# Optimization experiments

Measured on AMD Instinct MI355X. Metric: run time of the kernel, lower is better.

The kernel has to match this reference:

```python
import jax, jax.numpy as jnp
import numpy as np

N_NODES = 25000
N_EDGES = 400000
ATOM_DIM = 39
EDGE_DIM = 10
FP = 128


def setup_inputs() -> dict:
    key = jax.random.key(0)
    ks = iter(jax.random.split(key, 40))
    def rn(shape, scale=0.1):
        return (jax.random.normal(next(ks), shape, dtype=jnp.float32) * scale)
    inp = {
        'x': jax.random.normal(next(ks), (N_NODES, ATOM_DIM), dtype=jnp.float32),
        'edge_index': jax.random.randint(next(ks), (2, N_EDGES), 0, N_NODES, dtype=jnp.int32),
        'edge_attr': jax.random.normal(next(ks), (N_EDGES, EDGE_DIM), dtype=jnp.float32),
        # layer 0 (step=0): atom_fc + neighbor_fc + align/attend/GRU
        'l0_atom_fc_w': rn((FP, ATOM_DIM)), 'l0_atom_fc_b': rn((FP,)),
        'l0_neighbor_fc_w': rn((FP, ATOM_DIM + EDGE_DIM)), 'l0_neighbor_fc_b': rn((FP,)),
        'l0_align_w': rn((1, 2 * FP)), 'l0_align_b': rn((1,)),
        'l0_attend_w': rn((FP, FP)), 'l0_attend_b': rn((FP,)),
        'l0_w_ih': rn((3 * FP, FP)), 'l0_w_hh': rn((3 * FP, FP)),
        'l0_b_ih': rn((3 * FP,)), 'l0_b_hh': rn((3 * FP,)),
        # layer 1 (step=1): align/attend/GRU only
        'l1_align_w': rn((1, 2 * FP)), 'l1_align_b': rn((1,)),
        'l1_attend_w': rn((FP, FP)), 'l1_attend_b': rn((FP,)),
        'l1_w_ih': rn((3 * FP, FP)), 'l1_w_hh': rn((3 * FP, FP)),
        'l1_b_ih': rn((3 * FP,)), 'l1_b_hh': rn((3 * FP,)),
    }
    return inp


def _lrelu(v):
    return jax.nn.leaky_relu(v, negative_slope=0.01)


def _gru_cell(inp, h, w_ih, w_hh, b_ih, b_hh):
    # torch.nn.GRUCell math
    gi = inp @ w_ih.T + b_ih
    gh = h @ w_hh.T + b_hh
    i_r, i_z, i_n = jnp.split(gi, 3, axis=-1)
    h_r, h_z, h_n = jnp.split(gh, 3, axis=-1)
    r = jax.nn.sigmoid(i_r + h_r)
    z = jax.nn.sigmoid(i_z + h_z)
    n = jnp.tanh(i_n + r * h_n)
    return (1.0 - z) * n + z * h


def _segment_softmax(e, idx, num_segments):
    # PyG torch_geometric.utils.softmax: per-segment max-shifted exp / (sum + 1e-16)
    m = jax.ops.segment_max(e, idx, num_segments=num_segments)
    ex = jnp.exp(e - m[idx])
    s = jax.ops.segment_sum(ex, idx, num_segments=num_segments)
    return ex / (s[idx] + 1e-16)


def _edge_block(x_i, x_j, src, dst, n_nodes, aw, ab, tw, tb, w_ih, w_hh, b_ih, b_hh):
    # align -> segment softmax (keyed by source index, as in the torch code) -> attend -> GRU -> scatter-add
    evu = _lrelu(jnp.concatenate([x_i, x_j], axis=-1) @ aw.T + ab)      # [E,1]
    avu = _segment_softmax(evu, src, n_nodes)                            # [E,1]
    c = jax.nn.elu(avu * (x_i @ tw.T + tb))                              # [E,FP]; dropout is identity in eval
    h = _gru_cell(c, x_i, w_ih, w_hh, b_ih, b_hh)                        # [E,FP]
    return jax.ops.segment_sum(h, dst, num_segments=n_nodes)            # [N,FP] default 'add' aggregation


def reference(x, edge_index, edge_attr,
              l0_atom_fc_w, l0_atom_fc_b, l0_neighbor_fc_w, l0_neighbor_fc_b,
              l0_align_w, l0_align_b, l0_attend_w, l0_attend_b,
              l0_w_ih, l0_w_hh, l0_b_ih, l0_b_hh,
              l1_align_w, l1_align_b, l1_attend_w, l1_attend_b,
              l1_w_ih, l1_w_hh, l1_b_ih, l1_b_hh):
    src, dst = edge_index[0], edge_index[1]   # PyG flow source_to_target: x_j=x[src], x_i=x[dst]
    n_nodes = x.shape[0]
    # --- layer 0 (step == 0) ---
    x_i = _lrelu(x[dst] @ l0_atom_fc_w.T + l0_atom_fc_b)
    x_j = _lrelu(jnp.concatenate([x[src], edge_attr], axis=-1) @ l0_neighbor_fc_w.T + l0_neighbor_fc_b)
    x = _edge_block(x_i, x_j, src, dst, n_nodes,
                    l0_align_w, l0_align_b, l0_attend_w, l0_attend_b,
                    l0_w_ih, l0_w_hh, l0_b_ih, l0_b_hh)
    # --- layer 1 (step == 1) ---
    x_i = x[dst]
    x_j = x[src]
    x = _edge_block(x_i, x_j, src, dst, n_nodes,
                    l1_align_w, l1_align_b, l1_attend_w, l1_attend_b,
                    l1_w_ih, l1_w_hh, l1_b_ih, l1_b_hh)
    return x
```

## Files before the change

### kernel.cpp

```cpp
#include <hip/hip_runtime.h>
#include <math.h>

#define NN 25000
#define NE 400000
#define NINF -1e30f

typedef __attribute__((ext_vector_type(8))) short bf16x8;
typedef __attribute__((ext_vector_type(4))) float f32x4;

__device__ __forceinline__ float lrelu(float x){ return x > 0.f ? x : 0.01f*x; }
__device__ __forceinline__ float elu1(float x){ return x > 0.f ? x : (__expf(x)-1.f); }
__device__ __forceinline__ float sigm(float x){ return 1.f/(1.f+__expf(-x)); }
__device__ __forceinline__ float tanh_fast(float x){ float e=__expf(2.f*x); return 1.f - 2.f/(e+1.f); }
__device__ __forceinline__ short f2bf(float f){
    union { float f; unsigned u; } v; v.f = f;
    unsigned r = v.u + 0x7fff + ((v.u >> 16) & 1);
    return (short)(r >> 16);
}
__device__ __forceinline__ float bf2f(short s){
    union { unsigned u; float f; } v; v.u = ((unsigned)(unsigned short)s) << 16;
    return v.f;
}
__device__ __forceinline__ unsigned cvtpk_bf16(float lo, float hi){
    unsigned r;
    asm volatile("v_cvt_pk_bf16_f32 %0, %1, %2" : "=v"(r) : "v"(lo), "v"(hi));
    return r;
}

__global__ __launch_bounds__(256) void k_pack8(
    const float* __restrict__ w0, const float* __restrict__ w1,
    const float* __restrict__ w2, const float* __restrict__ w3,
    const float* __restrict__ w4, const float* __restrict__ w5,
    const float* __restrict__ w6, const float* __restrict__ w7,
    short* __restrict__ o0, short* __restrict__ o1, short* __restrict__ o2,
    short* __restrict__ o3, short* __restrict__ o4, short* __restrict__ o5,
    short* __restrict__ o6, short* __restrict__ o7)
{
    int b = blockIdx.x;
    if (b < 896){
        const float* w; short* o; int idx;
        if      (b < 192){ w=w0; o=o0; idx = b*256; }
        else if (b < 384){ w=w1; o=o1; idx = (b-192)*256; }
        else if (b < 576){ w=w2; o=o2; idx = (b-384)*256; }
        else if (b < 768){ w=w3; o=o3; idx = (b-576)*256; }
        else if (b < 832){ w=w4; o=o4; idx = (b-768)*256; }
        else             { w=w5; o=o5; idx = (b-832)*256; }
        idx += threadIdx.x;
        int i    = idx & 7;
        int lane = (idx >> 3) & 63;
        int ks   = (idx >> 9) & 3;
        int tile = idx >> 11;
        int row  = tile*16 + (lane & 15);
        int k    = ks*32 + ((lane >> 4) << 3) + i;
        o[idx] = f2bf(w[row*128 + k]);
    } else {
        const float* w; short* o; int idx; int pitch;
        if (b < 928){ w=w6; o=o6; idx = (b-896)*256; pitch = 39; }
        else        { w=w7; o=o7; idx = (b-928)*256; pitch = 49; }
        idx += threadIdx.x;
        int i    = idx & 7;
        int lane = (idx >> 3) & 63;
        int ks   = (idx >> 9) & 1;
        int tile = idx >> 10;
        int row  = tile*16 + (lane & 15);
        int k    = ks*32 + ((lane >> 4) << 3) + i;
        o[idx] = (k < 39) ? f2bf(w[row*pitch + k]) : (short)0;
    }
}

__global__ __launch_bounds__(256) void k_hist2(const int* __restrict__ src,
                                               const int* __restrict__ dst,
                                               unsigned* __restrict__ hd,
                                               unsigned* __restrict__ hs)
{
    int e = blockIdx.x*256 + threadIdx.x;
    if (e < NE){
        atomicAdd(&hd[dst[e]], 1u);
        atomicAdd(&hs[src[e]], 1u);
    }
}

__global__ __launch_bounds__(1024) void k_scan2(
    const unsigned* __restrict__ hd, unsigned* __restrict__ cd,
    const unsigned* __restrict__ hs, unsigned* __restrict__ cs,
    int* __restrict__ srcptr)
{
    __shared__ unsigned ps[1024];
    const int issrc = blockIdx.x;
    const unsigned* h = issrc ? hs : hd;
    unsigned* c = issrc ? cs : cd;
    const int t = threadIdx.x;
    unsigned loc[25]; unsigned sum = 0;
    const int base = t*25;
    #pragma unroll
    for (int i=0;i<25;i++){ int n=base+i; unsigned v=(n<NN)?h[n]:0u; loc[i]=sum; sum+=v; }
    ps[t]=sum; __syncthreads();
    for (int off=1; off<1024; off<<=1){
        unsigned v = (t>=off)? ps[t-off] : 0u;
        __syncthreads();
        ps[t] += v;
        __syncthreads();
    }
    unsigned bex = (t==0)? 0u : ps[t-1];
    #pragma unroll
    for (int i=0;i<25;i++){
        int n=base+i;
        if (n<NN){
            unsigned off = bex + loc[i];
            c[n] = off;
            if (issrc) srcptr[n] = (int)off;
        }
    }
    if (issrc && t==1023) srcptr[NN] = NE;
}

__global__ __launch_bounds__(256) void k_scatter2(
    const int* __restrict__ src, const int* __restrict__ dst,
    unsigned* __restrict__ cd, unsigned* __restrict__ cs,
    int* __restrict__ se_dst, int* __restrict__ inv_dst,
    int* __restrict__ se2_id, int* __restrict__ se2_dst)
{
    int e = blockIdx.x*256 + threadIdx.x;
    if (e < NE){
        int d = dst[e], s = src[e];
        unsigned p = atomicAdd(&cd[d], 1u);
        se_dst[p] = d;
        inv_dst[e] = (int)p;
        unsigned q = atomicAdd(&cs[s], 1u);
        se2_id[q] = e;
        se2_dst[q] = d;
    }
}

__global__ __launch_bounds__(512) void k_l0_prep(
    const float* __restrict__ x,
    const float* __restrict__ ba, const float* __restrict__ bn,
    const float* __restrict__ aw,
    const short* __restrict__ wap, const short* __restrict__ wnp,
    const short* __restrict__ twp, const float* __restrict__ tb,
    const short* __restrict__ whhp, const float* __restrict__ bhh,
    short* __restrict__ A16, short* __restrict__ B16, float* __restrict__ di,
    short* __restrict__ T16, short* __restrict__ GH16)
{
    __shared__ short x_lds[64*72];
    __shared__ __align__(16) char A_lds[64*272];
    const int t = threadIdx.x;
    const int base = blockIdx.x << 6;
    for (int idx = t; idx < 64*64; idx += 512){
        int r = idx >> 6, k = idx & 63;
        int node = base + r;
        float v = (k < 39 && node < NN) ? x[(size_t)node*39 + k] : 0.f;
        x_lds[r*72 + k] = f2bf(v);
    }
    __syncthreads();
    const int w = t >> 6, lane = t & 63;
    const int l15 = lane & 15, lhi = lane >> 4;
    const int jb = w*16 + l15;
    f32x4 Aacc[4], Bacc[4];
    #pragma unroll
    for (int m=0; m<4; ++m){ Aacc[m] = (f32x4){0,0,0,0}; Bacc[m] = (f32x4){0,0,0,0}; }
    #pragma unroll
    for (int ks=0; ks<2; ++ks){
        bf16x8 af[4];
        #pragma unroll
        for (int m=0; m<4; ++m)
            af[m] = *(const bf16x8*)&x_lds[(m*16+l15)*72 + ks*32 + lhi*8];
        bf16x8 wfA = *(const bf16x8*)(wap + (size_t)((w*2 + ks)*64 + lane)*8);
        bf16x8 wfB = *(const bf16x8*)(wnp + (size_t)((w*2 + ks)*64 + lane)*8);
        #pragma unroll
        for (int m=0; m<4; ++m){
            Aacc[m] = __builtin_amdgcn_mfma_f32_16x16x32_bf16(af[m], wfA, Aacc[m], 0, 0, 0);
            Bacc[m] = __builtin_amdgcn_mfma_f32_16x16x32_bf16(af[m], wfB, Bacc[m], 0, 0, 0);
        }
    }
    {
        float bav = ba[jb], bnv = bn[jb];
        #pragma unroll
        for (int m=0; m<4; ++m){
            #pragma unroll
            for (int reg=0; reg<4; ++reg){
                int e = m*16 + lhi*4 + reg;
                int node = base + e;
                float avv = lrelu(Aacc[m][reg] + bav);
                short ab16 = f2bf(avv);
                *(short*)(A_lds + e*272 + jb*2) = ab16;
                if (node < NN){
                    A16[(size_t)node*128 + jb] = ab16;
                    B16[(size_t)node*128 + jb] = f2bf(Bacc[m][reg] + bnv);
                }
            }
        }
    }
    __syncthreads();
    {
        float a0 = aw[lane], a1 = aw[64+lane];
        for (int i=0;i<8;++i){
            int r = w*8 + i;
            int node = base + r;
            float v0 = bf2f(*(const short*)(A_lds + r*272 + lane*2));
            float v1 = bf2f(*(const short*)(A_lds + r*272 + 128 + lane*2));
            float pa = v0*a0 + v1*a1;
            #pragma unroll
            for (int off=32; off; off>>=1) pa += __shfl_xor(pa, off);
            if (lane==0 && node<NN) di[node] = pa;
        }
    }
    f32x4 Tacc[4], gh[4][3];
    {
        float tbv = tb[jb];
        #pragma unroll
        for (int m=0; m<4; ++m) Tacc[m] = (f32x4){tbv, tbv, tbv, tbv};
        #pragma unroll
        for (int g=0; g<3; ++g){
            float bv = bhh[g*128 + jb];
            #pragma unroll
            for (int m=0; m<4; ++m) gh[m][g] = (f32x4){bv, bv, bv, bv};
        }
    }
    #pragma unroll
    for (int ks=0; ks<4; ++ks){
        bf16x8 af[4];
        #pragma unroll
        for (int m=0; m<4; ++m)
            af[m] = *(const bf16x8*)(A_lds + (m*16+l15)*272 + ks*64 + (lhi<<4));
        bf16x8 tf = *(const bf16x8*)(twp + (size_t)((w*4 + ks)*64 + lane)*8);
        #pragma unroll
        for (int m=0; m<4; ++m)
            Tacc[m] = __builtin_amdgcn_mfma_f32_16x16x32_bf16(af[m], tf, Tacc[m], 0, 0, 0);
        #pragma unroll
        for (int g=0; g<3; ++g){
            bf16x8 wf = *(const bf16x8*)(whhp + (size_t)(((g*8+w)*4 + ks)*64 + lane)*8);
            #pragma unroll
            for (int m=0; m<4; ++m)
                gh[m][g] = __builtin_amdgcn_mfma_f32_16x16x32_bf16(af[m], wf, gh[m][g], 0, 0, 0);
        }
    }
    #pragma unroll
    for (int m=0; m<4; ++m){
        #pragma unroll
        for (int reg=0; reg<4; ++reg){
            int node = base + m*16 + lhi*4 + reg;
            if (node < NN){
                T16[(size_t)node*128 + jb]        = f2bf(Tacc[m][reg]);
                GH16[(size_t)node*384 + jb]       = f2bf(gh[m][0][reg]);
                GH16[(size_t)node*384 + 128 + jb] = f2bf(gh[m][1][reg]);
                GH16[(size_t)node*384 + 256 + jb] = f2bf(gh[m][2][reg]);
            }
        }
    }
}

__global__ __launch_bounds__(512) void k_l1_prep(
    const float* __restrict__ out0, const float* __restrict__ aw,
    const short* __restrict__ twp, const float* __restrict__ tb,
    const short* __restrict__ whhp, const float* __restrict__ bhh,
    short* __restrict__ x16, float* __restrict__ di, float* __restrict__ dj,
    short* __restrict__ T16, short* __restrict__ GH16)
{
    __shared__ __align__(16) char x_lds[64*272];
    const int t = threadIdx.x;
    const int base = blockIdx.x << 6;
    {
        int r = t >> 3, c0 = (t & 7) * 16;
        int node = base + r;
        int nc = node < NN ? node : NN-1;
        const float4* sp = (const float4*)(out0 + (size_t)nc*128 + c0);
        float4 f0 = sp[0], f1 = sp[1], f2 = sp[2], f3 = sp[3];
        union { short s[16]; int4 v[2]; } u;
        u.s[0]=f2bf(f0.x); u.s[1]=f2bf(f0.y); u.s[2]=f2bf(f0.z); u.s[3]=f2bf(f0.w);
        u.s[4]=f2bf(f1.x); u.s[5]=f2bf(f1.y); u.s[6]=f2bf(f1.z); u.s[7]=f2bf(f1.w);
        u.s[8]=f2bf(f2.x); u.s[9]=f2bf(f2.y); u.s[10]=f2bf(f2.z); u.s[11]=f2bf(f2.w);
        u.s[12]=f2bf(f3.x); u.s[13]=f2bf(f3.y); u.s[14]=f2bf(f3.z); u.s[15]=f2bf(f3.w);
        *(int4*)(x_lds + r*272 + c0*2)      = u.v[0];
        *(int4*)(x_lds + r*272 + c0*2 + 16) = u.v[1];
        if (node < NN){
            *(int4*)(x16 + (size_t)node*128 + c0)     = u.v[0];
            *(int4*)(x16 + (size_t)node*128 + c0 + 8) = u.v[1];
        }
    }
    __syncthreads();
    const int w = t >> 6, lane = t & 63;
    {
        float a0 = aw[lane], a1 = aw[64+lane], a2 = aw[128+lane], a3 = aw[192+lane];
        for (int i=0;i<8;++i){
            int r = w*8 + i;
            int node = base + r;
            float v0 = bf2f(*(const short*)(x_lds + r*272 + lane*2));
            float v1 = bf2f(*(const short*)(x_lds + r*272 + 128 + lane*2));
            float pa = v0*a0 + v1*a1;
            float pb = v0*a2 + v1*a3;
            #pragma unroll
            for (int off=32; off; off>>=1){ pa += __shfl_xor(pa,off); pb += __shfl_xor(pb,off); }
            if (lane==0 && node<NN){ di[node]=pa; dj[node]=pb; }
        }
    }
    const int l15 = lane & 15, lhi = lane >> 4;
    const int jb = w*16 + l15;
    f32x4 Tacc[4], gh[4][3];
    {
        float tbv = tb[jb];
        #pragma unroll
        for (int m=0; m<4; ++m) Tacc[m] = (f32x4){tbv, tbv, tbv, tbv};
        #pragma unroll
        for (int g=0; g<3; ++g){
            float bv = bhh[g*128 + jb];
            #pragma unroll
            for (int m=0; m<4; ++m) gh[m][g] = (f32x4){bv, bv, bv, bv};
        }
    }
    #pragma unroll
    for (int ks=0; ks<4; ++ks){
        bf16x8 af[4];
        #pragma unroll
        for (int m=0; m<4; ++m)
            af[m] = *(const bf16x8*)(x_lds + (m*16+l15)*272 + ks*64 + (lhi<<4));
        bf16x8 tf = *(const bf16x8*)(twp + (size_t)((w*4 + ks)*64 + lane)*8);
        #pragma unroll
        for (int m=0; m<4; ++m)
            Tacc[m] = __builtin_amdgcn_mfma_f32_16x16x32_bf16(af[m], tf, Tacc[m], 0, 0, 0);
        #pragma unroll
        for (int g=0; g<3; ++g){
            bf16x8 wf = *(const bf16x8*)(whhp + (size_t)(((g*8+w)*4 + ks)*64 + lane)*8);
            #pragma unroll
            for (int m=0; m<4; ++m)
                gh[m][g] = __builtin_amdgcn_mfma_f32_16x16x32_bf16(af[m], wf, gh[m][g], 0, 0, 0);
        }
    }
    #pragma unroll
    for (int m=0; m<4; ++m){
        #pragma unroll
        for (int reg=0; reg<4; ++reg){
            int node = base + m*16 + lhi*4 + reg;
            if (node < NN){
                T16[(size_t)node*128 + jb]        = f2bf(Tacc[m][reg]);
                GH16[(size_t)node*384 + jb]       = f2bf(gh[m][0][reg]);
                GH16[(size_t)node*384 + 128 + jb] = f2bf(gh[m][1][reg]);
                GH16[(size_t)node*384 + 256 + jb] = f2bf(gh[m][2][reg]);
            }
        }
    }
}

__global__ __launch_bounds__(256) void k_align0(
    const int* __restrict__ srcptr, const int* __restrict__ se2_id,
    const int* __restrict__ se2_dst, const int* __restrict__ inv_dst,
    const float* __restrict__ ea, const short* __restrict__ B16,
    const float* __restrict__ wn, const float* __restrict__ aw,
    const float* __restrict__ ab, const float* __restrict__ di,
    float* __restrict__ evu_tmp, float* __restrict__ avu)
{
    const int lane = threadIdx.x & 63;
    const int node = blockIdx.x*4 + (threadIdx.x >> 6);
    if (node >= NN) return;
    const int start = srcptr[node], end = srcptr[node+1];
    if (start >= end) return;
    float wn2a[10], wn2b[10];
    #pragma unroll
    for (int k=0;k<10;++k){
        wn2a[k] = wn[lane*49 + 39 + k];
        wn2b[k] = wn[(lane+64)*49 + 39 + k];
    }
    const float awa = aw[128+lane], awb = aw[192+lane];
    const float abv = ab[0];
    const float v1b = bf2f(B16[(size_t)node*128 + lane]);
    const float v2b = bf2f(B16[(size_t)node*128 + 64 + lane]);
    const int deg = end - start;
    if (deg <= 64){
        int myeid = 0; float mydi = 0.f; float ear[10];
        if (lane < deg){
            int pos = start + lane;
            myeid = se2_id[pos];
            mydi  = di[se2_dst[pos]];
            #pragma unroll
            for (int k=0;k<10;++k) ear[k] = ea[(size_t)myeid*10 + k];
        }
        float pv = NINF;
        for (int i=0;i<deg;++i){
            float v1 = v1b, v2 = v2b;
            #pragma unroll
            for (int k=0;k<10;++k){
                float e = __shfl(ear[k], i);
                v1 += e*wn2a[k]; v2 += e*wn2b[k];
            }
            v1 = lrelu(v1); v2 = lrelu(v2);
            float p = v1*awa + v2*awb;
            #pragma unroll
            for (int off=32; off; off>>=1) p += __shfl_xor(p, off);
            float pe = lrelu(p + __shfl(mydi, i) + abv);
            if (lane == i) pv = pe;
        }
        float cm = pv;
        #pragma unroll
        for (int off=32; off; off>>=1) cm = fmaxf(cm, __shfl_xor(cm, off));
        float ex = (lane < deg) ? __expf(pv - cm) : 0.f;
        float cs = ex;
        #pragma unroll
        for (int off=32; off; off>>=1) cs += __shfl_xor(cs, off);
        if (lane < deg) avu[inv_dst[myeid]] = ex / (cs + 1e-16f);
    } else {
        float mrun = NINF, srun = 0.f;
        for (int c0 = start; c0 < end; c0 += 64){
            int nE = min(64, end - c0);
            int myeid=0; float mydi=0.f; float ear[10];
            if (lane < nE){
                int pos = c0 + lane;
                myeid = se2_id[pos];
                mydi = di[se2_dst[pos]];
                #pragma unroll
                for (int k=0;k<10;++k) ear[k] = ea[(size_t)myeid*10 + k];
            }
            float pv = NINF;
            for (int i=0;i<nE;++i){
                float v1=v1b, v2=v2b;
                #pragma unroll
                for (int k=0;k<10;++k){
                    float e = __shfl(ear[k], i);
                    v1 += e*wn2a[k]; v2 += e*wn2b[k];
                }
                v1=lrelu(v1); v2=lrelu(v2);
                float p = v1*awa + v2*awb;
                #pragma unroll
                for (int off=32; off; off>>=1) p += __shfl_xor(p, off);
                float pe = lrelu(p + __shfl(mydi,i) + abv);
                if (lane == i) pv = pe;
            }
            if (lane < nE) evu_tmp[c0+lane] = pv;
            float cm = pv;
            #pragma unroll
            for (int off=32; off; off>>=1) cm = fmaxf(cm, __shfl_xor(cm,off));
            float nm = fmaxf(mrun, cm);
            float exs = (lane<nE)? __expf(pv-nm) : 0.f;
            float cs = exs;
            #pragma unroll
            for (int off=32; off; off>>=1) cs += __shfl_xor(cs, off);
            srun = srun*__expf(mrun-nm) + cs;
            mrun = nm;
        }
        float inv = 1.f/(srun + 1e-16f);
        for (int c0 = start; c0 < end; c0 += 64){
            int nE = min(64, end - c0);
            if (lane < nE){
                int pos = c0+lane;
                float pv = evu_tmp[pos];
                avu[inv_dst[se2_id[pos]]] = __expf(pv - mrun)*inv;
            }
        }
    }
}

__global__ __launch_bounds__(256) void k_align1(
    const int* __restrict__ srcptr, const int* __restrict__ se2_id,
    const int* __restrict__ se2_dst, const int* __restrict__ inv_dst,
    const float* __restrict__ di, const float* __restrict__ dj,
    const float* __restrict__ ab,
    float* __restrict__ evu_tmp, float* __restrict__ avu)
{
    const int lane = threadIdx.x & 63;
    const int node = blockIdx.x*4 + (threadIdx.x >> 6);
    if (node >= NN) return;
    const int start = srcptr[node], end = srcptr[node+1];
    if (start >= end) return;
    const float djs = dj[node] + ab[0];
    const int deg = end - start;
    if (deg <= 64){
        int myeid = 0; float pv = NINF;
        if (lane < deg){
            int pos = start + lane;
            myeid = se2_id[pos];
            pv = lrelu(di[se2_dst[pos]] + djs);
        }
        float cm = pv;
        #pragma unroll
        for (int off=32; off; off>>=1) cm = fmaxf(cm, __shfl_xor(cm, off));
        float ex = (lane < deg) ? __expf(pv - cm) : 0.f;
        float cs = ex;
        #pragma unroll
        for (int off=32; off; off>>=1) cs += __shfl_xor(cs, off);
        if (lane < deg) avu[inv_dst[myeid]] = ex / (cs + 1e-16f);
    } else {
        float mrun = NINF, srun = 0.f;
        for (int c0 = start; c0 < end; c0 += 64){
            int nE = min(64, end - c0);
            float pv = NINF;
            if (lane < nE){
                int pos = c0 + lane;
                pv = lrelu(di[se2_dst[pos]] + djs);
                evu_tmp[pos] = pv;
            }
            float cm = pv;
            #pragma unroll
            for (int off=32; off; off>>=1) cm = fmaxf(cm, __shfl_xor(cm,off));
            float nm = fmaxf(mrun, cm);
            float exs = (lane<nE)? __expf(pv-nm) : 0.f;
            float cs = exs;
            #pragma unroll
            for (int off=32; off; off>>=1) cs += __shfl_xor(cs, off);
            srun = srun*__expf(mrun-nm) + cs;
            mrun = nm;
        }
        float inv = 1.f/(srun + 1e-16f);
        for (int c0 = start; c0 < end; c0 += 64){
            int nE = min(64, end - c0);
            if (lane < nE){
                int pos = c0+lane;
                avu[inv_dst[se2_id[pos]]] = __expf(evu_tmp[pos] - mrun)*inv;
            }
        }
    }
}

__global__ __launch_bounds__(512) void k_edge_gru(
    const int* __restrict__ se_dst,
    const float* __restrict__ avu,
    const short* __restrict__ T16, const short* __restrict__ GH16,
    const short* __restrict__ HP16,
    const short* __restrict__ wihp, const float* __restrict__ bih,
    float* __restrict__ out)
{
    __shared__ __align__(16) char smem[17536];
    __shared__ __align__(16) int dsts[64];
    __shared__ float av[64];
    char* const c_lds = smem;
    const int t = threadIdx.x;
    const int p0 = blockIdx.x << 6;
    if (t < 64){
        dsts[t] = se_dst[p0 + t];
        av[t] = avu[p0 + t];
    }
    __syncthreads();
    #pragma unroll
    for (int it=0; it<2; ++it){
        int cid = it*512 + t;
        int row = cid >> 4, ch = cid & 15;
        int d = dsts[row];
        float a = av[row];
        bf16x8 tv = *(const bf16x8*)(T16 + (size_t)d*128 + ch*8);
        float c0 = elu1(a*bf2f(tv[0])), c1 = elu1(a*bf2f(tv[1]));
        float c2 = elu1(a*bf2f(tv[2])), c3 = elu1(a*bf2f(tv[3]));
        float c4 = elu1(a*bf2f(tv[4])), c5 = elu1(a*bf2f(tv[5]));
        float c6 = elu1(a*bf2f(tv[6])), c7 = elu1(a*bf2f(tv[7]));
        int4 pk;
        pk.x = (int)cvtpk_bf16(c0, c1);
        pk.y = (int)cvtpk_bf16(c2, c3);
        pk.z = (int)cvtpk_bf16(c4, c5);
        pk.w = (int)cvtpk_bf16(c6, c7);
        *(int4*)(c_lds + row*272 + ch*16) = pk;
    }
    __syncthreads();
    const int w = t >> 6, lane = t & 63;
    const int l15 = lane & 15, lhi = lane >> 4;
    const int jb = w*16 + l15;
    f32x4 gi[4][3];
    #pragma unroll
    for (int g=0; g<3; ++g){
        float bv = bih[g*128 + jb];
        #pragma unroll
        for (int m=0; m<4; ++m) gi[m][g] = (f32x4){bv, bv, bv, bv};
    }
    #pragma unroll
    for (int ks=0; ks<4; ++ks){
        bf16x8 cf[4];
        #pragma unroll
        for (int m=0; m<4; ++m)
            cf[m] = *(const bf16x8*)(c_lds + (m*16+l15)*272 + ks*64 + (lhi<<4));
        #pragma unroll
        for (int g=0; g<3; ++g){
            bf16x8 wf = *(const bf16x8*)(wihp + (size_t)(((g*8+w)*4 + ks)*64 + lane)*8);
            #pragma unroll
            for (int m=0; m<4; ++m)
                gi[m][g] = __builtin_amdgcn_mfma_f32_16x16x32_bf16(cf[m], wf, gi[m][g], 0, 0, 0);
        }
    }
    float hreg[4][4];
    {
        int dprev = -1;
        float ghr=0.f, ghz=0.f, ghn=0.f, hp=0.f;
        #pragma unroll
        for (int m=0; m<4; ++m){
            int4 dv = *(const int4*)&dsts[m*16 + lhi*4];
            int dd[4] = {dv.x, dv.y, dv.z, dv.w};
            #pragma unroll
            for (int reg=0; reg<4; ++reg){
                int d = dd[reg];
                if (d != dprev){
                    const short* gh = GH16 + (size_t)d*384 + jb;
                    ghr = bf2f(gh[0]);
                    ghz = bf2f(gh[128]);
                    ghn = bf2f(gh[256]);
                    hp  = bf2f(HP16[(size_t)d*128 + jb]);
                    dprev = d;
                }
                float r = sigm(gi[m][0][reg] + ghr);
                float z = sigm(gi[m][1][reg] + ghz);
                float n = tanh_fast(gi[m][2][reg] + r*ghn);
                hreg[m][reg] = (1.f - z)*n + z*hp;
            }
        }
    }
    float* hlds = (float*)smem;
    #pragma unroll
    for (int half=0; half<2; ++half){
        __syncthreads();
        #pragma unroll
        for (int m=half*2; m<half*2+2; ++m){
            #pragma unroll
            for (int reg=0; reg<4; ++reg){
                int e = m*16 + lhi*4 + reg;
                hlds[(e - half*32)*137 + jb] = hreg[m][reg];
            }
        }
        __syncthreads();
        {
            const int j = t & 127, eg = t >> 7;
            float acc = 0.f; int prev = -1;
            #pragma unroll
            for (int k=0; k<8; ++k){
                int r = eg*8 + k;
                int d = dsts[half*32 + r];
                float v = hlds[r*137 + j];
                if (d == prev) acc += v;
                else {
                    if (prev >= 0) atomicAdd(out + (size_t)prev*128 + j, acc);
                    acc = v; prev = d;
                }
            }
            atomicAdd(out + (size_t)prev*128 + j, acc);
        }
    }
}

extern "C" void kernel_launch(void* const* d_in, const int* in_sizes, int n_in,
                              void* d_out, int out_size, void* d_ws, size_t ws_size,
                              hipStream_t stream) {
    const float* x    = (const float*)d_in[0];
    const int*   eidx = (const int*)d_in[1];
    const int*   esrc = eidx;
    const int*   edst = eidx + NE;
    const float* ea   = (const float*)d_in[2];
    const float* a_w  = (const float*)d_in[3];
    const float* a_b  = (const float*)d_in[4];
    const float* n_w  = (const float*)d_in[5];
    const float* n_b  = (const float*)d_in[6];
    const float* al_w0= (const float*)d_in[7];
    const float* al_b0= (const float*)d_in[8];
    const float* t_w0 = (const float*)d_in[9];
    const float* t_b0 = (const float*)d_in[10];
    const float* wih0 = (const float*)d_in[11];
    const float* whh0 = (const float*)d_in[12];
    const float* bih0 = (const float*)d_in[13];
    const float* bhh0 = (const float*)d_in[14];
    const float* al_w1= (const float*)d_in[15];
    const float* al_b1= (const float*)d_in[16];
    const float* t_w1 = (const float*)d_in[17];
    const float* t_b1 = (const float*)d_in[18];
    const float* wih1 = (const float*)d_in[19];
    const float* whh1 = (const float*)d_in[20];
    const float* bih1 = (const float*)d_in[21];
    const float* bhh1 = (const float*)d_in[22];

    float* ws   = (float*)d_ws;
    float* out0 = ws;
    float* avu  = out0 + (size_t)NN*128;
    float* evu_tmp = avu + NE;
    float* di   = evu_tmp + NE;
    float* dj   = di + NN;
    unsigned* hist_d = (unsigned*)(dj + NN);
    unsigned* hist_s = hist_d + NN;
    unsigned* cur_d  = hist_s + NN;
    unsigned* cur_s  = cur_d + NN;
    int* srcptr = (int*)(cur_s + NN);
    int* se_dst  = srcptr + NN + 1;
    int* inv_dst = se_dst + NE;
    int* se2_id  = inv_dst + NE;
    int* se2_dst = se2_id + NE;
    short* A16  = (short*)(se2_dst + NE);
    short* BX16 = A16 + (size_t)NN*128;
    short* T16  = BX16 + (size_t)NN*128;
    short* GH16 = T16 + (size_t)NN*128;
    short* wp0  = GH16 + (size_t)NN*384;
    short* wp1  = wp0 + 49152;
    short* wh0p = wp1 + 49152;
    short* wh1p = wh0p + 49152;
    short* tp0  = wh1p + 49152;
    short* tp1  = tp0 + 16384;
    short* wap  = tp1 + 16384;
    short* wnp  = wap + 8192;

    hipMemsetAsync(out0, 0, (size_t)NN*128*sizeof(float), stream);
    hipMemsetAsync(d_out, 0, (size_t)NN*128*sizeof(float), stream);
    hipMemsetAsync(hist_d, 0, (size_t)2*NN*sizeof(unsigned), stream);

    dim3 blk(256);
    k_pack8<<<dim3(960), blk, 0, stream>>>(wih0, wih1, whh0, whh1, t_w0, t_w1, a_w, n_w,
                                           wp0, wp1, wh0p, wh1p, tp0, tp1, wap, wnp);
    k_hist2<<<dim3((NE+255)/256), blk, 0, stream>>>(esrc, edst, hist_d, hist_s);
    k_scan2<<<dim3(2), dim3(1024), 0, stream>>>(hist_d, cur_d, hist_s, cur_s, srcptr);
    k_scatter2<<<dim3((NE+255)/256), blk, 0, stream>>>(esrc, edst, cur_d, cur_s,
                                                       se_dst, inv_dst, se2_id, se2_dst);
    k_l0_prep<<<dim3((NN+63)/64), dim3(512), 0, stream>>>(x, a_b, n_b, al_w0, wap, wnp,
                                                          tp0, t_b0, wh0p, bhh0,
                                                          A16, BX16, di, T16, GH16);
    k_align0<<<dim3((NN+3)/4), blk, 0, stream>>>(srcptr, se2_id, se2_dst, inv_dst,
                                                 ea, BX16, n_w, al_w0, al_b0, di, evu_tmp, avu);
    k_edge_gru<<<dim3(NE/64), dim3(512), 0, stream>>>(se_dst, avu, T16, GH16, A16,
                                                      wp0, bih0, out0);
    k_l1_prep<<<dim3((NN+63)/64), dim3(512), 0, stream>>>(out0, al_w1, tp1, t_b1, wh1p, bhh1,
                                                          BX16, di, dj, T16, GH16);
    k_align1<<<dim3((NN+3)/4), blk, 0, stream>>>(srcptr, se2_id, se2_dst, inv_dst,
                                                 di, dj, al_b1, evu_tmp, avu);
    k_edge_gru<<<dim3(NE/64), dim3(512), 0, stream>>>(se_dst, avu, T16, GH16, BX16,
                                                      wp1, bih1, (float*)d_out);
}
```

Measured before the change: 673.9 us.

## Fuse setup kernels, fold output zeroing into prep, simplify GRU epilogue

Merges weight packing with the edge histogram into one launch. Folds the edge scatter and the zeroing of both output buffers into extra blocks of the layer-0 prep kernel, which removes two memsets and two launches. The edge GRU epilogue now loads GH/HP per edge without reuse caching and writes all 64 edges to a larger LDS buffer in one pass with a single reduction pass, cutting barriers. In exchange it uses more LDS, which may lower occupancy, and does redundant global loads for repeated destinations.

Result: faster. 607.1 us (median of 2 runs) (-9.9%).

```diff
diff --git a/kernel.cpp b/kernel.cpp
--- a/kernel.cpp
+++ b/kernel.cpp
@@ -23,18 +23,20 @@
 }
 __device__ __forceinline__ unsigned cvtpk_bf16(float lo, float hi){
     unsigned r;
-    asm volatile("v_cvt_pk_bf16_f32 %0, %1, %2" : "=v"(r) : "v"(lo), "v"(hi));
+    asm("v_cvt_pk_bf16_f32 %0, %1, %2" : "=v"(r) : "v"(lo), "v"(hi));
     return r;
 }
 
-__global__ __launch_bounds__(256) void k_pack8(
+__global__ __launch_bounds__(256) void k_setup(
     const float* __restrict__ w0, const float* __restrict__ w1,
     const float* __restrict__ w2, const float* __restrict__ w3,
     const float* __restrict__ w4, const float* __restrict__ w5,
     const float* __restrict__ w6, const float* __restrict__ w7,
     short* __restrict__ o0, short* __restrict__ o1, short* __restrict__ o2,
     short* __restrict__ o3, short* __restrict__ o4, short* __restrict__ o5,
-    short* __restrict__ o6, short* __restrict__ o7)
+    short* __restrict__ o6, short* __restrict__ o7,
+    const int* __restrict__ src, const int* __restrict__ dst,
+    unsigned* __restrict__ hd, unsigned* __restrict__ hs)
 {
     int b = blockIdx.x;
     if (b < 896){
@@ -53,7 +55,7 @@
         int row  = tile*16 + (lane & 15);
         int k    = ks*32 + ((lane >> 4) << 3) + i;
         o[idx] = f2bf(w[row*128 + k]);
-    } else {
+    } else if (b < 960){
         const float* w; short* o; int idx; int pitch;
         if (b < 928){ w=w6; o=o6; idx = (b-896)*256; pitch = 39; }
         else        { w=w7; o=o7; idx = (b-928)*256; pitch = 49; }
@@ -65,18 +67,12 @@
         int row  = tile*16 + (lane & 15);
         int k    = ks*32 + ((lane >> 4) << 3) + i;
         o[idx] = (k < 39) ? f2bf(w[row*pitch + k]) : (short)0;
-    }
-}
-
-__global__ __launch_bounds__(256) void k_hist2(const int* __restrict__ src,
-                                               const int* __restrict__ dst,
-                                               unsigned* __restrict__ hd,
-                                               unsigned* __restrict__ hs)
-{
-    int e = blockIdx.x*256 + threadIdx.x;
-    if (e < NE){
-        atomicAdd(&hd[dst[e]], 1u);
-        atomicAdd(&hs[src[e]], 1u);
+    } else {
+        int e = (b-960)*256 + threadIdx.x;
+        if (e < NE){
+            atomicAdd(&hd[dst[e]], 1u);
+            atomicAdd(&hs[src[e]], 1u);
+        }
     }
 }
 
@@ -114,25 +110,7 @@
     if (issrc && t==1023) srcptr[NN] = NE;
 }
 
-__global__ __launch_bounds__(256) void k_scatter2(
-    const int* __restrict__ src, const int* __restrict__ dst,
-    unsigned* __restrict__ cd, unsigned* __restrict__ cs,
-    int* __restrict__ se_dst, int* __restrict__ inv_dst,
-    int* __restrict__ se2_id, int* __restrict__ se2_dst)
-{
-    int e = blockIdx.x*256 + threadIdx.x;
-    if (e < NE){
-        int d = dst[e], s = src[e];
-        unsigned p = atomicAdd(&cd[d], 1u);
-        se_dst[p] = d;
-        inv_dst[e] = (int)p;
-        unsigned q = atomicAdd(&cs[s], 1u);
-        se2_id[q] = e;
-        se2_dst[q] = d;
-    }
-}
-
-__global__ __launch_bounds__(512) void k_l0_prep(
+__global__ __launch_bounds__(512) void k_big(
     const float* __restrict__ x,
     const float* __restrict__ ba, const float* __restrict__ bn,
     const float* __restrict__ aw,
@@ -140,12 +118,36 @@
     const short* __restrict__ twp, const float* __restrict__ tb,
     const short* __restrict__ whhp, const float* __restrict__ bhh,
     short* __restrict__ A16, short* __restrict__ B16, float* __restrict__ di,
-    short* __restrict__ T16, short* __restrict__ GH16)
+    short* __restrict__ T16, short* __restrict__ GH16,
+    const int* __restrict__ src, const int* __restrict__ dst,
+    unsigned* __restrict__ cd, unsigned* __restrict__ cs,
+    int* __restrict__ se_dst, int* __restrict__ inv_dst,
+    int* __restrict__ se2_id, int* __restrict__ se2_dst,
+    float* __restrict__ out0z, float* __restrict__ doutz)
 {
     __shared__ short x_lds[64*72];
     __shared__ __align__(16) char A_lds[64*272];
     const int t = threadIdx.x;
-    const int base = blockIdx.x << 6;
+    const int b = blockIdx.x;
+    if (b >= 391){
+        int e = (b-391)*512 + t;
+        if (e < NE){
+            float4 z = {0.f,0.f,0.f,0.f};
+            *(float4*)(out0z + (size_t)e*8)     = z;
+            *(float4*)(out0z + (size_t)e*8 + 4) = z;
+            *(float4*)(doutz + (size_t)e*8)     = z;
+            *(float4*)(doutz + (size_t)e*8 + 4) = z;
+            int d = dst[e], s = src[e];
+            unsigned p = atomicAdd(&cd[d], 1u);
+            se_dst[p] = d;
+            inv_dst[e] = (int)p;
+            unsigned q = atomicAdd(&cs[s], 1u);
+            se2_id[q] = e;
+            se2_dst[q] = d;
+        }
+        return;
+    }
+    const int base = b << 6;
     for (int idx = t; idx < 64*64; idx += 512){
         int r = idx >> 6, k = idx & 63;
         int node = base + r;
@@ -517,8 +519,8 @@
     const short* __restrict__ wihp, const float* __restrict__ bih,
     float* __restrict__ out)
 {
-    __shared__ __align__(16) char smem[17536];
-    __shared__ __align__(16) int dsts[64];
+    __shared__ __align__(16) char smem[64*132*4];
+    __shared__ int dsts[64];
     __shared__ float av[64];
     char* const c_lds = smem;
     const int t = threadIdx.x;
@@ -572,60 +574,49 @@
         }
     }
     float hreg[4][4];
+    #pragma unroll
+    for (int m=0; m<4; ++m){
+        #pragma unroll
+        for (int reg=0; reg<4; ++reg){
+            int e = m*16 + lhi*4 + reg;
+            int d = dsts[e];
+            const short* gh = GH16 + (size_t)d*384;
+            float r = sigm(gi[m][0][reg] + bf2f(gh[jb]));
+            float z = sigm(gi[m][1][reg] + bf2f(gh[128+jb]));
+            float n = tanh_fast(gi[m][2][reg] + r*bf2f(gh[256+jb]));
+            float hp = bf2f(HP16[(size_t)d*128 + jb]);
+            hreg[m][reg] = (1.f - z)*n + z*hp;
+        }
+    }
+    __syncthreads();
     {
-        int dprev = -1;
-        float ghr=0.f, ghz=0.f, ghn=0.f, hp=0.f;
+        float* hlds = (float*)smem;
         #pragma unroll
         for (int m=0; m<4; ++m){
-            int4 dv = *(const int4*)&dsts[m*16 + lhi*4];
-            int dd[4] = {dv.x, dv.y, dv.z, dv.w};
-            #pragma unroll
-            for (int reg=0; reg<4; ++reg){
-                int d = dd[reg];
-                if (d != dprev){
-                    const short* gh = GH16 + (size_t)d*384 + jb;
-                    ghr = bf2f(gh[0]);
-                    ghz = bf2f(gh[128]);
-                    ghn = bf2f(gh[256]);
-                    hp  = bf2f(HP16[(size_t)d*128 + jb]);
-                    dprev = d;
-                }
-                float r = sigm(gi[m][0][reg] + ghr);
-                float z = sigm(gi[m][1][reg] + ghz);
-                float n = tanh_fast(gi[m][2][reg] + r*ghn);
-                hreg[m][reg] = (1.f - z)*n + z*hp;
-            }
-        }
-    }
-    float* hlds = (float*)smem;
-    #pragma unroll
-    for (int half=0; half<2; ++half){
-        __syncthreads();
-        #pragma unroll
-        for (int m=half*2; m<half*2+2; ++m){
             #pragma unroll
             for (int reg=0; reg<4; ++reg){
                 int e = m*16 + lhi*4 + reg;
-                hlds[(e - half*32)*137 + jb] = hreg[m][reg];
-            }
-        }
-        __syncthreads();
-        {
-            const int j = t & 127, eg = t >> 7;
-            float acc = 0.f; int prev = -1;
-            #pragma unroll
-            for (int k=0; k<8; ++k){
-                int r = eg*8 + k;
-                int d = dsts[half*32 + r];
-                float v = hlds[r*137 + j];
-                if (d == prev) acc += v;
-                else {
-                    if (prev >= 0) atomicAdd(out + (size_t)prev*128 + j, acc);
-                    acc = v; prev = d;
-                }
-            }
-            atomicAdd(out + (size_t)prev*128 + j, acc);
-        }
+                hlds[e*132 + jb] = hreg[m][reg];
+            }
+        }
+    }
+    __syncthreads();
+    {
+        const int j = t & 127, eg = t >> 7;
+        const float* hlds = (const float*)smem;
+        float acc = 0.f; int prev = -1;
+        #pragma unroll
+        for (int el=0; el<16; ++el){
+            int e = eg*16 + el;
+            int d = dsts[e];
+            float v = hlds[e*132 + j];
+            if (d == prev) acc += v;
+            else {
+                if (prev >= 0) atomicAdd(out + (size_t)prev*128 + j, acc);
+                acc = v; prev = d;
+            }
+        }
+        atomicAdd(out + (size_t)prev*128 + j, acc);
     }
 }
 
@@ -666,10 +657,10 @@
     float* dj   = di + NN;
     unsigned* hist_d = (unsigned*)(dj + NN);
     unsigned* hist_s = hist_d + NN;
-    unsigned* cur_d  = hist_s + NN;
+    int* srcptr = (int*)(hist_s + NN);
+    unsigned* cur_d  = (unsigned*)(srcptr + NN + 1);
     unsigned* cur_s  = cur_d + NN;
-    int* srcptr = (int*)(cur_s + NN);
-    int* se_dst  = srcptr + NN + 1;
+    int* se_dst  = (int*)(cur_s + NN);
     int* inv_dst = se_dst + NE;
     int* se2_id  = inv_dst + NE;
     int* se2_dst = se2_id + NE;
@@ -686,27 +677,25 @@
     short* wap  = tp1 + 16384;
     short* wnp  = wap + 8192;
 
-    hipMemsetAsync(out0, 0, (size_t)NN*128*sizeof(float), stream);
-    hipMemsetAsync(d_out, 0, (size_t)NN*128*sizeof(float), stream);
     hipMemsetAsync(hist_d, 0, (size_t)2*NN*sizeof(unsigned), stream);
 
-    dim3 blk(256);
-    k_pack8<<<dim3(960), blk, 0, stream>>>(wih0, wih1, whh0, whh1, t_w0, t_w1, a_w, n_w,
-                                           wp0, wp1, wh0p, wh1p, tp0, tp1, wap, wnp);
-    k_hist2<<<dim3((NE+255)/256), blk, 0, stream>>>(esrc, edst, hist_d, hist_s);
+    k_setup<<<dim3(960 + (NE+255)/256), dim3(256), 0, stream>>>(
+        wih0, wih1, whh0, whh1, t_w0, t_w1, a_w, n_w,
+        wp0, wp1, wh0p, wh1p, tp0, tp1, wap, wnp,
+        esrc, edst, hist_d, hist_s);
     k_scan2<<<dim3(2), dim3(1024), 0, stream>>>(hist_d, cur_d, hist_s, cur_s, srcptr);
-    k_scatter2<<<dim3((NE+255)/256), blk, 0, stream>>>(esrc, edst, cur_d, cur_s,
-                                                       se_dst, inv_dst, se2_id, se2_dst);
-    k_l0_prep<<<dim3((NN+63)/64), dim3(512), 0, stream>>>(x, a_b, n_b, al_w0, wap, wnp,
-                                                          tp0, t_b0, wh0p, bhh0,
-                                                          A16, BX16, di, T16, GH16);
-    k_align0<<<dim3((NN+3)/4), blk, 0, stream>>>(srcptr, se2_id, se2_dst, inv_dst,
+    k_big<<<dim3(391 + (NE+511)/512), dim3(512), 0, stream>>>(
+        x, a_b, n_b, al_w0, wap, wnp, tp0, t_b0, wh0p, bhh0,
+        A16, BX16, di, T16, GH16,
+        esrc, edst, cur_d, cur_s, se_dst, inv_dst, se2_id, se2_dst,
+        out0, (float*)d_out);
+    k_align0<<<dim3((NN+3)/4), dim3(256), 0, stream>>>(srcptr, se2_id, se2_dst, inv_dst,
                                                  ea, BX16, n_w, al_w0, al_b0, di, evu_tmp, avu);
     k_edge_gru<<<dim3(NE/64), dim3(512), 0, stream>>>(se_dst, avu, T16, GH16, A16,
                                                       wp0, bih0, out0);
     k_l1_prep<<<dim3((NN+63)/64), dim3(512), 0, stream>>>(out0, al_w1, tp1, t_b1, wh1p, bhh1,
                                                           BX16, di, dj, T16, GH16);
-    k_align1<<<dim3((NN+3)/4), blk, 0, stream>>>(srcptr, se2_id, se2_dst, inv_dst,
+    k_align1<<<dim3((NN+3)/4), dim3(256), 0, stream>>>(srcptr, se2_id, se2_dst, inv_dst,
                                                  di, dj, al_b1, evu_tmp, avu);
     k_edge_gru<<<dim3(NE/64), dim3(512), 0, stream>>>(se_dst, avu, T16, GH16, BX16,
                                                       wp1, bih1, (float*)d_out);
```
